# Kernel optimization log

Hardware: AMD Instinct MI355X
Metric: run time of the kernel (lower is better)

The kernel has to match this reference:

```python
import jax, jax.numpy as jnp
from jax import lax
import numpy as np

STATE_DIM, LATENT_DIM, HIDDEN_DIM = 18, 3, 16
BN_EPS = 1e-5


def _xavier(key, out_dim, in_dim):
    a = (6.0 / (in_dim + out_dim)) ** 0.5
    return jax.random.uniform(key, (out_dim, in_dim), minval=-a, maxval=a, dtype=jnp.float32)


def setup_inputs() -> dict:
    key = jax.random.key(0)
    ks = jax.random.split(key, 12)
    B, S, T = 4096, 256, 64
    inp = {
        "x_sequence": jax.random.normal(ks[0], (B, S, STATE_DIM), dtype=jnp.float32),
        "t_span": jnp.linspace(0.0, 6.3, T, dtype=jnp.float32),
        # encoder: Linear(18->16), ReLU, (Dropout off), BatchNorm1d(16, eval), Linear(16->3)
        "enc_w1": _xavier(ks[1], HIDDEN_DIM, STATE_DIM), "enc_b1": jnp.zeros((HIDDEN_DIM,), jnp.float32),
        "enc_bn_g": jnp.ones((HIDDEN_DIM,), jnp.float32), "enc_bn_b": jnp.zeros((HIDDEN_DIM,), jnp.float32),
        "enc_bn_m": jnp.zeros((HIDDEN_DIM,), jnp.float32), "enc_bn_v": jnp.ones((HIDDEN_DIM,), jnp.float32),
        "enc_w2": _xavier(ks[2], LATENT_DIM, HIDDEN_DIM), "enc_b2": jnp.zeros((LATENT_DIM,), jnp.float32),
        # decoder: Linear(3->16), ReLU, BN(16, eval), Linear(16->18)
        "dec_w1": _xavier(ks[3], HIDDEN_DIM, LATENT_DIM), "dec_b1": jnp.zeros((HIDDEN_DIM,), jnp.float32),
        "dec_bn_g": jnp.ones((HIDDEN_DIM,), jnp.float32), "dec_bn_b": jnp.zeros((HIDDEN_DIM,), jnp.float32),
        "dec_bn_m": jnp.zeros((HIDDEN_DIM,), jnp.float32), "dec_bn_v": jnp.ones((HIDDEN_DIM,), jnp.float32),
        "dec_w2": _xavier(ks[4], STATE_DIM, HIDDEN_DIM), "dec_b2": jnp.zeros((STATE_DIM,), jnp.float32),
        # ode_func: Linear(3->8), Tanh, Linear(8->3)
        "ode_w1": _xavier(ks[5], HIDDEN_DIM // 2, LATENT_DIM), "ode_b1": jnp.zeros((HIDDEN_DIM // 2,), jnp.float32),
        "ode_w2": _xavier(ks[6], LATENT_DIM, HIDDEN_DIM // 2), "ode_b2": jnp.zeros((LATENT_DIM,), jnp.float32),
        # perturbation classifier: Linear(3->4), ReLU, Linear(4->1), Sigmoid
        "cls_w1": _xavier(ks[7], 4, LATENT_DIM), "cls_b1": jnp.zeros((4,), jnp.float32),
        "cls_w2": _xavier(ks[8], 1, 4), "cls_b2": jnp.zeros((1,), jnp.float32),
    }
    return inp


def _bn_eval(x, g, b, m, v):
    return (x - m) * (g / jnp.sqrt(v + BN_EPS)) + b


def reference(x_sequence, t_span,
              enc_w1, enc_b1, enc_bn_g, enc_bn_b, enc_bn_m, enc_bn_v, enc_w2, enc_b2,
              dec_w1, dec_b1, dec_bn_g, dec_bn_b, dec_bn_m, dec_bn_v, dec_w2, dec_b2,
              ode_w1, ode_b1, ode_w2, ode_b2,
              cls_w1, cls_b1, cls_w2, cls_b2):
    B, S, D = x_sequence.shape
    T = t_span.shape[0]

    def encode(x):  # [N, 18] -> [N, 3]
        h = jax.nn.relu(x @ enc_w1.T + enc_b1)
        h = _bn_eval(h, enc_bn_g, enc_bn_b, enc_bn_m, enc_bn_v)
        return h @ enc_w2.T + enc_b2

    def decode(z):  # [N, 3] -> [N, 18]
        h = jax.nn.relu(z @ dec_w1.T + dec_b1)
        h = _bn_eval(h, dec_bn_g, dec_bn_b, dec_bn_m, dec_bn_v)
        return h @ dec_w2.T + dec_b2

    def ode_func(z):  # [B, 3] -> [B, 3]
        return jnp.tanh(z @ ode_w1.T + ode_b1) @ ode_w2.T + ode_b2

    x_flat = x_sequence.reshape(-1, D)              # [B*S, 18]
    z_flat = encode(x_flat)                         # [B*S, 3]
    z_seq = z_flat.reshape(B, S, LATENT_DIM)
    z0 = z_seq[:, -1, :]                            # [B, 3]

    # explicit Euler integration: z <- z + 0.1 * f(z), T steps
    def step(z, _):
        z_next = z + 0.1 * ode_func(z)
        return z_next, z_next

    _, z_traj = lax.scan(step, z0, None, length=T)  # [T, B, 3]
    z_pred = jnp.transpose(z_traj, (1, 0, 2))       # [B, T, 3]

    x_recon = decode(z_flat).reshape(B, S, D)
    x_pred = decode(z_pred.reshape(-1, LATENT_DIM)).reshape(B, T, D)

    z_mean = jnp.mean(z_seq, axis=1)                # [B, 3]
    h = jax.nn.relu(z_mean @ cls_w1.T + cls_b1)
    perturbation_prob = jax.nn.sigmoid(h @ cls_w2.T + cls_b2)  # [B, 1]

    return (x_recon, x_pred, perturbation_prob, z_seq)
```

## Files before the change

kernel.cpp:

```cpp
#include <hip/hip_runtime.h>
#include <math.h>

constexpr int Bn = 4096, Sn = 256, Tn = 64;
constexpr int Dn = 18, Hn = 16, Ln = 3;
constexpr float EPS = 1e-5f;

constexpr size_t OFF_XP   = (size_t)Bn * Sn * Dn;
constexpr size_t OFF_PROB = OFF_XP + (size_t)Bn * Tn * Dn;
constexpr size_t OFF_ZS   = OFF_PROB + (size_t)Bn;

__device__ __forceinline__ float fast_tanh(float x) {
    float ax = fabsf(x);
    float e  = __expf(-2.0f * ax);
    float r  = (1.0f - e) / (1.0f + e);
    return copysignf(r, x);
}

__global__ __launch_bounds__(256) void k1_encdec(
    const float* __restrict__ x,
    const float* __restrict__ ew1, const float* __restrict__ eb1,
    const float* __restrict__ eg,  const float* __restrict__ ebb,
    const float* __restrict__ em,  const float* __restrict__ ev,
    const float* __restrict__ ew2, const float* __restrict__ eb2,
    const float* __restrict__ dw1, const float* __restrict__ db1,
    const float* __restrict__ dg,  const float* __restrict__ dbn,
    const float* __restrict__ dm,  const float* __restrict__ dv,
    const float* __restrict__ dw2, const float* __restrict__ db2,
    const float* __restrict__ cw1, const float* __restrict__ cb1,
    const float* __restrict__ cw2, const float* __restrict__ cb2,
    float* __restrict__ xrec, float* __restrict__ prob, float* __restrict__ zseq)
{
    const int b = blockIdx.x;
    const int s = threadIdx.x;
    const size_t row = (size_t)b * Sn + s;

    __shared__ float esc[Hn], esh[Hn], dsc[Hn], dsh[Hn];
    if (s < Hn) {
        float sc = eg[s] / sqrtf(ev[s] + EPS);
        esc[s] = sc; esh[s] = ebb[s] - em[s] * sc;
        float sd = dg[s] / sqrtf(dv[s] + EPS);
        dsc[s] = sd; dsh[s] = dbn[s] - dm[s] * sd;
    }
    __syncthreads();

    float xv[Dn];
    const float2* xp = reinterpret_cast<const float2*>(x + row * Dn);
    #pragma unroll
    for (int i = 0; i < Dn / 2; ++i) { float2 t = xp[i]; xv[2*i] = t.x; xv[2*i+1] = t.y; }

    float h[Hn];
    #pragma unroll
    for (int j = 0; j < Hn; ++j) {
        float a = eb1[j];
        #pragma unroll
        for (int k = 0; k < Dn; ++k) a = fmaf(ew1[j*Dn + k], xv[k], a);
        a = fmaxf(a, 0.0f);
        h[j] = fmaf(a, esc[j], esh[j]);
    }
    float z0 = eb2[0], z1 = eb2[1], z2 = eb2[2];
    #pragma unroll
    for (int j = 0; j < Hn; ++j) {
        z0 = fmaf(ew2[0*Hn + j], h[j], z0);
        z1 = fmaf(ew2[1*Hn + j], h[j], z1);
        z2 = fmaf(ew2[2*Hn + j], h[j], z2);
    }
    float* zp = zseq + row * Ln;
    zp[0] = z0; zp[1] = z1; zp[2] = z2;

    float h2[Hn];
    #pragma unroll
    for (int j = 0; j < Hn; ++j) {
        float a = fmaf(dw1[j*Ln + 0], z0, db1[j]);
        a = fmaf(dw1[j*Ln + 1], z1, a);
        a = fmaf(dw1[j*Ln + 2], z2, a);
        a = fmaxf(a, 0.0f);
        h2[j] = fmaf(a, dsc[j], dsh[j]);
    }
    float2* op = reinterpret_cast<float2*>(xrec + row * Dn);
    #pragma unroll
    for (int i = 0; i < Dn / 2; ++i) {
        float a0 = db2[2*i], a1 = db2[2*i + 1];
        #pragma unroll
        for (int j = 0; j < Hn; ++j) {
            a0 = fmaf(dw2[(2*i)*Hn + j],   h2[j], a0);
            a1 = fmaf(dw2[(2*i+1)*Hn + j], h2[j], a1);
        }
        op[i] = make_float2(a0, a1);
    }

    float r0 = z0, r1 = z1, r2 = z2;
    #pragma unroll
    for (int off = 32; off > 0; off >>= 1) {
        r0 += __shfl_down(r0, off);
        r1 += __shfl_down(r1, off);
        r2 += __shfl_down(r2, off);
    }
    __shared__ float red[4][3];
    const int lane = s & 63, wid = s >> 6;
    if (lane == 0) { red[wid][0] = r0; red[wid][1] = r1; red[wid][2] = r2; }
    __syncthreads();
    if (s == 0) {
        float m0 = (red[0][0] + red[1][0] + red[2][0] + red[3][0]) * (1.0f / Sn);
        float m1 = (red[0][1] + red[1][1] + red[2][1] + red[3][1]) * (1.0f / Sn);
        float m2 = (red[0][2] + red[1][2] + red[2][2] + red[3][2]) * (1.0f / Sn);
        float logit = cb2[0];
        #pragma unroll
        for (int j = 0; j < 4; ++j) {
            float a = fmaf(cw1[j*3 + 0], m0, cb1[j]);
            a = fmaf(cw1[j*3 + 1], m1, a);
            a = fmaf(cw1[j*3 + 2], m2, a);
            a = fmaxf(a, 0.0f);
            logit = fmaf(cw2[j], a, logit);
        }
        prob[b] = 1.0f / (1.0f + __expf(-logit));
    }
}

__global__ __launch_bounds__(256) void k2_ode(
    const float* __restrict__ zseq,
    const float* __restrict__ ow1, const float* __restrict__ ob1,
    const float* __restrict__ ow2, const float* __restrict__ ob2,
    float* __restrict__ scratch)
{
    const int b = blockIdx.x * blockDim.x + threadIdx.x;
    const float* zp = zseq + ((size_t)b * Sn + (Sn - 1)) * Ln;
    float z0 = zp[0], z1 = zp[1], z2 = zp[2];

    float w1[8][3], bb1[8], w2v[3][8], bb2[3];
    #pragma unroll
    for (int j = 0; j < 8; ++j) {
        bb1[j] = ob1[j];
        #pragma unroll
        for (int k = 0; k < 3; ++k) w1[j][k] = ow1[j*3 + k];
    }
    #pragma unroll
    for (int i = 0; i < 3; ++i) {
        bb2[i] = ob2[i];
        #pragma unroll
        for (int j = 0; j < 8; ++j) w2v[i][j] = ow2[i*8 + j];
    }

    float* op = scratch + (size_t)b * Tn * Dn;
    for (int t = 0; t < Tn; ++t) {
        float a[8];
        #pragma unroll
        for (int j = 0; j < 8; ++j) {
            float u = fmaf(w1[j][0], z0, bb1[j]);
            u = fmaf(w1[j][1], z1, u);
            u = fmaf(w1[j][2], z2, u);
            a[j] = fast_tanh(u);
        }
        float d0 = bb2[0], d1 = bb2[1], d2 = bb2[2];
        #pragma unroll
        for (int j = 0; j < 8; ++j) {
            d0 = fmaf(w2v[0][j], a[j], d0);
            d1 = fmaf(w2v[1][j], a[j], d1);
            d2 = fmaf(w2v[2][j], a[j], d2);
        }
        z0 = fmaf(0.1f, d0, z0);
        z1 = fmaf(0.1f, d1, z1);
        z2 = fmaf(0.1f, d2, z2);
        op[t*Dn + 0] = z0; op[t*Dn + 1] = z1; op[t*Dn + 2] = z2;
    }
}

__global__ __launch_bounds__(256) void k3_decpred(
    const float* __restrict__ dw1, const float* __restrict__ db1,
    const float* __restrict__ dg,  const float* __restrict__ dbn,
    const float* __restrict__ dm,  const float* __restrict__ dv,
    const float* __restrict__ dw2, const float* __restrict__ db2,
    float* xpred)
{
    const int r = blockIdx.x * blockDim.x + threadIdx.x;

    __shared__ float dsc[Hn], dsh[Hn];
    if (threadIdx.x < Hn) {
        float sd = dg[threadIdx.x] / sqrtf(dv[threadIdx.x] + EPS);
        dsc[threadIdx.x] = sd;
        dsh[threadIdx.x] = dbn[threadIdx.x] - dm[threadIdx.x] * sd;
    }
    __syncthreads();

    float* rowp = xpred + (size_t)r * Dn;
    float z0 = rowp[0], z1 = rowp[1], z2 = rowp[2];

    float h2[Hn];
    #pragma unroll
    for (int j = 0; j < Hn; ++j) {
        float a = fmaf(dw1[j*Ln + 0], z0, db1[j]);
        a = fmaf(dw1[j*Ln + 1], z1, a);
        a = fmaf(dw1[j*Ln + 2], z2, a);
        a = fmaxf(a, 0.0f);
        h2[j] = fmaf(a, dsc[j], dsh[j]);
    }
    float2* op = reinterpret_cast<float2*>(rowp);
    #pragma unroll
    for (int i = 0; i < Dn / 2; ++i) {
        float a0 = db2[2*i], a1 = db2[2*i + 1];
        #pragma unroll
        for (int j = 0; j < Hn; ++j) {
            a0 = fmaf(dw2[(2*i)*Hn + j],   h2[j], a0);
            a1 = fmaf(dw2[(2*i+1)*Hn + j], h2[j], a1);
        }
        op[i] = make_float2(a0, a1);
    }
}

extern "C" void kernel_launch(void* const* d_in, const int* in_sizes, int n_in,
                              void* d_out, int out_size, void* d_ws, size_t ws_size,
                              hipStream_t stream)
{
    const float* x   = (const float*)d_in[0];
    const float* ew1 = (const float*)d_in[2];
    const float* eb1 = (const float*)d_in[3];
    const float* eg  = (const float*)d_in[4];
    const float* ebb = (const float*)d_in[5];
    const float* em  = (const float*)d_in[6];
    const float* ev  = (const float*)d_in[7];
    const float* ew2 = (const float*)d_in[8];
    const float* eb2 = (const float*)d_in[9];
    const float* dw1 = (const float*)d_in[10];
    const float* db1 = (const float*)d_in[11];
    const float* dg  = (const float*)d_in[12];
    const float* dbn = (const float*)d_in[13];
    const float* dm  = (const float*)d_in[14];
    const float* dv  = (const float*)d_in[15];
    const float* dw2 = (const float*)d_in[16];
    const float* db2 = (const float*)d_in[17];
    const float* ow1 = (const float*)d_in[18];
    const float* ob1 = (const float*)d_in[19];
    const float* ow2 = (const float*)d_in[20];
    const float* ob2 = (const float*)d_in[21];
    const float* cw1 = (const float*)d_in[22];
    const float* cb1 = (const float*)d_in[23];
    const float* cw2 = (const float*)d_in[24];
    const float* cb2 = (const float*)d_in[25];

    float* out   = (float*)d_out;
    float* xrec  = out;
    float* xpred = out + OFF_XP;
    float* prob  = out + OFF_PROB;
    float* zseq  = out + OFF_ZS;

    k1_encdec<<<dim3(Bn), dim3(Sn), 0, stream>>>(
        x, ew1, eb1, eg, ebb, em, ev, ew2, eb2,
        dw1, db1, dg, dbn, dm, dv, dw2, db2,
        cw1, cb1, cw2, cb2, xrec, prob, zseq);

    k2_ode<<<dim3(Bn / 256), dim3(256), 0, stream>>>(
        zseq, ow1, ob1, ow2, ob2, xpred);

    k3_decpred<<<dim3((Bn * Tn) / 256), dim3(256), 0, stream>>>(
        dw1, db1, dg, dbn, dm, dv, dw2, db2, xpred);
}
```

Before: 276.2 us.

## Stage encoder I/O through LDS for coalesced loads/stores and use compact ODE scratch

The encoder kernel now loads each block's 256x18 input tile into shared memory with coalesced float4 reads, and writes the reconstruction back through shared memory with float4 stores. Before this, each thread read or wrote a 72-byte strided row. The ODE kernel writes its trajectory to a compact [T,B,3] scratch in workspace when space allows, and the prediction decoder reads from it and stores its output through LDS as well. The aim is better DRAM coalescing on this bandwidth-bound workload. The cost is 18KB of LDS per block, which may limit occupancy, and extra barriers.

```diff
diff --git a/kernel.cpp b/kernel.cpp
--- a/kernel.cpp
+++ b/kernel.cpp
@@ -32,21 +32,29 @@
 {
     const int b = blockIdx.x;
     const int s = threadIdx.x;
-    const size_t row = (size_t)b * Sn + s;
-
+    constexpr int TILE_F  = Sn * Dn;
+    constexpr int TILE_F4 = TILE_F / 4;
+
+    __shared__ float xt[TILE_F];
     __shared__ float esc[Hn], esh[Hn], dsc[Hn], dsh[Hn];
+    __shared__ float red[4][3];
+
     if (s < Hn) {
         float sc = eg[s] / sqrtf(ev[s] + EPS);
         esc[s] = sc; esh[s] = ebb[s] - em[s] * sc;
         float sd = dg[s] / sqrtf(dv[s] + EPS);
         dsc[s] = sd; dsh[s] = dbn[s] - dm[s] * sd;
     }
+
+    const float4* xg  = reinterpret_cast<const float4*>(x + (size_t)b * TILE_F);
+    float4*       xt4 = reinterpret_cast<float4*>(xt);
+    #pragma unroll
+    for (int i = s; i < TILE_F4; i += 256) xt4[i] = xg[i];
     __syncthreads();
 
     float xv[Dn];
-    const float2* xp = reinterpret_cast<const float2*>(x + row * Dn);
-    #pragma unroll
-    for (int i = 0; i < Dn / 2; ++i) { float2 t = xp[i]; xv[2*i] = t.x; xv[2*i+1] = t.y; }
+    #pragma unroll
+    for (int k = 0; k < Dn; ++k) xv[k] = xt[s * Dn + k];
 
     float h[Hn];
     #pragma unroll
@@ -64,7 +72,7 @@
         z1 = fmaf(ew2[1*Hn + j], h[j], z1);
         z2 = fmaf(ew2[2*Hn + j], h[j], z2);
     }
-    float* zp = zseq + row * Ln;
+    float* zp = zseq + ((size_t)b * Sn + s) * Ln;
     zp[0] = z0; zp[1] = z1; zp[2] = z2;
 
     float h2[Hn];
@@ -76,17 +84,18 @@
         a = fmaxf(a, 0.0f);
         h2[j] = fmaf(a, dsc[j], dsh[j]);
     }
-    float2* op = reinterpret_cast<float2*>(xrec + row * Dn);
-    #pragma unroll
-    for (int i = 0; i < Dn / 2; ++i) {
-        float a0 = db2[2*i], a1 = db2[2*i + 1];
-        #pragma unroll
-        for (int j = 0; j < Hn; ++j) {
-            a0 = fmaf(dw2[(2*i)*Hn + j],   h2[j], a0);
-            a1 = fmaf(dw2[(2*i+1)*Hn + j], h2[j], a1);
-        }
-        op[i] = make_float2(a0, a1);
-    }
+    #pragma unroll
+    for (int m = 0; m < Dn; ++m) {
+        float a = db2[m];
+        #pragma unroll
+        for (int j = 0; j < Hn; ++j) a = fmaf(dw2[m*Hn + j], h2[j], a);
+        xt[s * Dn + m] = a;
+    }
+    __syncthreads();
+
+    float4* og = reinterpret_cast<float4*>(xrec + (size_t)b * TILE_F);
+    #pragma unroll
+    for (int i = s; i < TILE_F4; i += 256) og[i] = xt4[i];
 
     float r0 = z0, r1 = z1, r2 = z2;
     #pragma unroll
@@ -95,7 +104,6 @@
         r1 += __shfl_down(r1, off);
         r2 += __shfl_down(r2, off);
     }
-    __shared__ float red[4][3];
     const int lane = s & 63, wid = s >> 6;
     if (lane == 0) { red[wid][0] = r0; red[wid][1] = r1; red[wid][2] = r2; }
     __syncthreads();
@@ -120,7 +128,7 @@
     const float* __restrict__ zseq,
     const float* __restrict__ ow1, const float* __restrict__ ob1,
     const float* __restrict__ ow2, const float* __restrict__ ob2,
-    float* __restrict__ scratch)
+    float* __restrict__ zscr, int zlayout)
 {
     const int b = blockIdx.x * blockDim.x + threadIdx.x;
     const float* zp = zseq + ((size_t)b * Sn + (Sn - 1)) * Ln;
@@ -140,7 +148,6 @@
         for (int j = 0; j < 8; ++j) w2v[i][j] = ow2[i*8 + j];
     }
 
-    float* op = scratch + (size_t)b * Tn * Dn;
     for (int t = 0; t < Tn; ++t) {
         float a[8];
         #pragma unroll
@@ -160,7 +167,9 @@
         z0 = fmaf(0.1f, d0, z0);
         z1 = fmaf(0.1f, d1, z1);
         z2 = fmaf(0.1f, d2, z2);
-        op[t*Dn + 0] = z0; op[t*Dn + 1] = z1; op[t*Dn + 2] = z2;
+        size_t idx = (zlayout == 0) ? ((size_t)t * Bn + b) * Ln
+                                    : ((size_t)b * Tn + t) * Dn;
+        zscr[idx + 0] = z0; zscr[idx + 1] = z1; zscr[idx + 2] = z2;
     }
 }
 
@@ -169,20 +178,27 @@
     const float* __restrict__ dg,  const float* __restrict__ dbn,
     const float* __restrict__ dm,  const float* __restrict__ dv,
     const float* __restrict__ dw2, const float* __restrict__ db2,
-    float* xpred)
+    const float* __restrict__ zscr, int zlayout,
+    float* __restrict__ xpred)
 {
     const int r = blockIdx.x * blockDim.x + threadIdx.x;
-
+    const int s = threadIdx.x;
+    constexpr int TILE_F  = 256 * Dn;
+    constexpr int TILE_F4 = TILE_F / 4;
+
+    __shared__ float ot[TILE_F];
     __shared__ float dsc[Hn], dsh[Hn];
-    if (threadIdx.x < Hn) {
-        float sd = dg[threadIdx.x] / sqrtf(dv[threadIdx.x] + EPS);
-        dsc[threadIdx.x] = sd;
-        dsh[threadIdx.x] = dbn[threadIdx.x] - dm[threadIdx.x] * sd;
-    }
-    __syncthreads();
-
-    float* rowp = xpred + (size_t)r * Dn;
-    float z0 = rowp[0], z1 = rowp[1], z2 = rowp[2];
+    if (s < Hn) {
+        float sd = dg[s] / sqrtf(dv[s] + EPS);
+        dsc[s] = sd;
+        dsh[s] = dbn[s] - dm[s] * sd;
+    }
+    __syncthreads();
+
+    const int bb = r / Tn, tt = r % Tn;
+    size_t zidx = (zlayout == 0) ? ((size_t)tt * Bn + bb) * Ln
+                                 : (size_t)r * Dn;
+    float z0 = zscr[zidx + 0], z1 = zscr[zidx + 1], z2 = zscr[zidx + 2];
 
     float h2[Hn];
     #pragma unroll
@@ -193,17 +209,19 @@
         a = fmaxf(a, 0.0f);
         h2[j] = fmaf(a, dsc[j], dsh[j]);
     }
-    float2* op = reinterpret_cast<float2*>(rowp);
-    #pragma unroll
-    for (int i = 0; i < Dn / 2; ++i) {
-        float a0 = db2[2*i], a1 = db2[2*i + 1];
-        #pragma unroll
-        for (int j = 0; j < Hn; ++j) {
-            a0 = fmaf(dw2[(2*i)*Hn + j],   h2[j], a0);
-            a1 = fmaf(dw2[(2*i+1)*Hn + j], h2[j], a1);
-        }
-        op[i] = make_float2(a0, a1);
-    }
+    #pragma unroll
+    for (int m = 0; m < Dn; ++m) {
+        float a = db2[m];
+        #pragma unroll
+        for (int j = 0; j < Hn; ++j) a = fmaf(dw2[m*Hn + j], h2[j], a);
+        ot[s * Dn + m] = a;
+    }
+    __syncthreads();
+
+    float4* og = reinterpret_cast<float4*>(xpred + (size_t)blockIdx.x * TILE_F);
+    const float4* ot4 = reinterpret_cast<const float4*>(ot);
+    #pragma unroll
+    for (int i = s; i < TILE_F4; i += 256) og[i] = ot4[i];
 }
 
 extern "C" void kernel_launch(void* const* d_in, const int* in_sizes, int n_in,
@@ -242,14 +260,19 @@
     float* prob  = out + OFF_PROB;
     float* zseq  = out + OFF_ZS;
 
+    const size_t zbytes = (size_t)Bn * Tn * Ln * sizeof(float);
+    float* zscr; int zlayout;
+    if (ws_size >= zbytes) { zscr = (float*)d_ws; zlayout = 0; }
+    else                   { zscr = xpred;        zlayout = 1; }
+
     k1_encdec<<<dim3(Bn), dim3(Sn), 0, stream>>>(
         x, ew1, eb1, eg, ebb, em, ev, ew2, eb2,
         dw1, db1, dg, dbn, dm, dv, dw2, db2,
         cw1, cb1, cw2, cb2, xrec, prob, zseq);
 
     k2_ode<<<dim3(Bn / 256), dim3(256), 0, stream>>>(
-        zseq, ow1, ob1, ow2, ob2, xpred);
+        zseq, ow1, ob1, ow2, ob2, zscr, zlayout);
 
     k3_decpred<<<dim3((Bn * Tn) / 256), dim3(256), 0, stream>>>(
-        dw1, db1, dg, dbn, dm, dv, dw2, db2, xpred);
-}
+        dw1, db1, dg, dbn, dm, dv, dw2, db2, zscr, zlayout, xpred);
+}
```

New measurement: 262.4 us. 5.0% less time.
